# Performance work log

Measured on AMD Instinct MI355X. Metric: run time of the kernel, lower is better.

## Reference

```python
import jax, jax.numpy as jnp
import numpy as np

N = 2048; C_IN = 2; H = 32; EMB = 16; OUT = 1; HORIZON = 12
B = 32; T = 16

def setup_inputs() -> dict:
    key = jax.random.key(0)
    ks = jax.random.split(key, 10)
    s = 0.05
    return {
        "x":  jax.random.normal(ks[0], (B, T, N, C_IN), dtype=jnp.float32),
        "E1": jax.random.normal(ks[1], (N, EMB), dtype=jnp.float32) * 0.1,
        "E2": jax.random.normal(ks[2], (N, EMB), dtype=jnp.float32) * 0.1,
        "Wx": jax.random.normal(ks[3], (C_IN, 4 * H), dtype=jnp.float32) * s,
        "bx": jnp.zeros((4 * H,), dtype=jnp.float32),
        "Wh": jax.random.normal(ks[4], (H, 4 * H), dtype=jnp.float32) * s,
        "bh": jnp.zeros((4 * H,), dtype=jnp.float32),
        "Wp": jax.random.normal(ks[5], (H, OUT * HORIZON), dtype=jnp.float32) * s,
        "bp": jnp.zeros((OUT * HORIZON,), dtype=jnp.float32),
    }

def reference(x, E1, E2, Wx, bx, Wh, bh, Wp, bp):
    Bb, Tt, Nn, _ = x.shape
    # adaptive adjacency: softmax(relu(E1 @ E2^T)) over last dim  [N,N]
    A = jax.nn.softmax(jax.nn.relu(E1 @ E2.T), axis=-1)

    def step(carry, xt):
        h, c = carry  # [B,N,H]
        # fused graph-conv gates: (A @ xt) Wx + (A @ h) Wh + biases -> [B,N,4H]
        gates = (jnp.einsum('ij,bjc->bic', A, xt) @ Wx + bx
                 + jnp.einsum('ij,bjh->bih', A, h) @ Wh + bh)
        i, f, o, g = jnp.split(gates, 4, axis=-1)
        i = jax.nn.sigmoid(i); f = jax.nn.sigmoid(f); o = jax.nn.sigmoid(o)
        g = jnp.tanh(g)
        c_t = f * c + i * g
        h_t = o * jnp.tanh(c_t)
        return (h_t, c_t), None

    h0 = jnp.zeros((Bb, Nn, H), dtype=x.dtype)
    c0 = jnp.zeros((Bb, Nn, H), dtype=x.dtype)
    (h_last, _), _ = jax.lax.scan(step, (h0, c0), jnp.transpose(x, (1, 0, 2, 3)))
    out = h_last @ Wp + bp                      # [B,N,horizon*out]
    out = out.reshape(Bb, Nn, HORIZON, OUT)
    return jnp.transpose(out, (0, 2, 1, 3))     # [B,horizon,N,out]
```

## Files before the change

kernel.cpp:

```cpp
#include <hip/hip_runtime.h>
#include <hip/hip_bf16.h>
#include <cstddef>
#include <cstdint>

#define NN 2048
#define CIN 2
#define HH 32
#define EMB 16
#define HOR 12
#define BB 32
#define TT 16
#define GC 128
#define XCOLS 1024
#define HCOLS 1024

#define ATILE_STRIDE 65536
#define BTILE_STRIDE 32768
#define LOPLANE 2097152

typedef __attribute__((ext_vector_type(8))) _Float16 f16x8;
typedef __attribute__((ext_vector_type(16))) float f32x16;

__device__ __forceinline__ void load_lds16(const void* g, void* l) {
    __builtin_amdgcn_global_load_lds(
        (const __attribute__((address_space(1))) void*)g,
        (__attribute__((address_space(3))) void*)l, 16, 0, 0);
}

__global__ __launch_bounds__(256) void e2_transpose(const float* __restrict__ E2,
                                                    float* __restrict__ E2T) {
    const int idx = blockIdx.x * 256 + threadIdx.x;
    const int k = idx >> 11;
    const int j = idx & 2047;
    E2T[idx] = E2[j * EMB + k];
}

__global__ __launch_bounds__(256) void precompute(const float* __restrict__ E1,
                                                  const float* __restrict__ E2T,
                                                  const float* __restrict__ x,
                                                  const float* __restrict__ Wx,
                                                  const float* __restrict__ bx,
                                                  const float* __restrict__ Wh,
                                                  const float* __restrict__ bh,
                                                  _Float16* __restrict__ A2,
                                                  _Float16* __restrict__ B2x,
                                                  _Float16* __restrict__ W16,
                                                  float* __restrict__ Wxr,
                                                  float* __restrict__ bfold) {
    const int blk = blockIdx.x;
    const int tid = threadIdx.x;

    if (blk < 512) {
        const int i = blk * 4 + (tid >> 6);
        const int l = tid & 63;
        float e1[EMB];
#pragma unroll
        for (int k = 0; k < EMB; ++k) e1[k] = E1[i * EMB + k];

        float s[32];
#pragma unroll
        for (int c = 0; c < 32; ++c) s[c] = 0.f;
#pragma unroll
        for (int k = 0; k < EMB; ++k) {
            const float ek = e1[k];
            const float* p = E2T + k * 2048 + l;
#pragma unroll
            for (int c = 0; c < 32; ++c) s[c] = fmaf(ek, p[c * 64], s[c]);
        }
        float mx = 0.f;
#pragma unroll
        for (int c = 0; c < 32; ++c) { s[c] = fmaxf(s[c], 0.f); mx = fmaxf(mx, s[c]); }
#pragma unroll
        for (int off = 32; off > 0; off >>= 1) mx = fmaxf(mx, __shfl_xor(mx, off, 64));
        float sum = 0.f;
#pragma unroll
        for (int c = 0; c < 32; ++c) { s[c] = expf(s[c] - mx); sum += s[c]; }
#pragma unroll
        for (int off = 32; off > 0; off >>= 1) sum += __shfl_xor(sum, off, 64);
        const float inv = 1.0f / sum;
        const int chb = (l >> 3);
        const int e   = l & 7;
#pragma unroll
        for (int c = 0; c < 32; ++c)
            A2[((size_t)(c * 8 + chb) * 2048 + i) * 8 + e] = (_Float16)(s[c] * inv);
    } else if (blk < 512 + 1024) {
        const int idx = (blk - 512) * 256 + tid;
        const int col = idx & 1023;
        const int jc  = idx >> 10;
        const int bt  = col >> 1;
        const int c   = col & 1;
        const float* xp = x + ((size_t)bt * NN + jc * 8) * CIN + c;
        f16x8 vh, vl;
#pragma unroll
        for (int e = 0; e < 8; ++e) {
            const float v = xp[e * CIN];
            const _Float16 hi = (_Float16)v;
            vh[e] = hi;
            vl[e] = (_Float16)(v - (float)hi);
        }
        const size_t base = ((size_t)jc * 1024 + col) * 8;
        *(f16x8*)(B2x + base) = vh;
        *(f16x8*)(B2x + base + LOPLANE) = vl;
    } else {
#pragma unroll
        for (int r = 0; r < 32; ++r) {
            const int idx = r * 256 + tid;
            const int e  = idx & 7;
            const int ln = (idx >> 3) & 63;
            const int gq = (idx >> 9) & 3;
            const int kh = (idx >> 11) & 1;
            const int k  = kh * 16 + (ln >> 5) * 8 + e;
            const int ch = gq * 32 + (ln & 31);
            const float v = Wh[k * GC + (ch & 3) * HH + (ch >> 2)];
            const _Float16 hi = (_Float16)v;
            W16[idx] = hi;
            W16[8192 + idx] = (_Float16)(v - (float)hi);
        }
        {
            const int idx = tid;
            const int c = idx >> 7, rem = idx & 127;
            const int h = rem >> 2, g = rem & 3;
            Wxr[idx] = Wx[c * GC + g * HH + h];
        }
        if (tid < 128) {
            const int h = tid >> 2, g = tid & 3;
            bfold[tid] = bx[g * HH + h] + bh[g * HH + h];
        }
    }
}

template <int NPROD, int GATE>
__global__ __launch_bounds__(512, 2) void gemm_fused(const _Float16* __restrict__ A2,
                                                     const _Float16* __restrict__ B2,
                                                     float* __restrict__ Cout,
                                                     const float* __restrict__ AX,
                                                     const _Float16* __restrict__ W16,
                                                     const float* __restrict__ Wxr,
                                                     const float* __restrict__ bfold,
                                                     float* __restrict__ cst,
                                                     float* __restrict__ h32,
                                                     _Float16* __restrict__ hTout,
                                                     int t, int last) {
    constexpr int SUBS   = (NPROD == 1) ? 2 : 1;
    constexpr int NT     = 64 / SUBS;
    constexpr int SUBBUF = 4096 + NPROD * 8192;
    constexpr int BUF    = SUBS * SUBBUF;
    constexpr int NBUF   = (NPROD == 1) ? 4 : 6;
    constexpr int PCH    = 256 + NPROD * 512;
    constexpr int NG     = (SUBS * PCH) / 64;
    constexpr int GMAX   = 3;
    constexpr int STAGE_SZ = NBUF * BUF;
    constexpr int SMEMSZ = GATE ? (STAGE_SZ + 1024 + 512 + 2048) : STAGE_SZ;
    __shared__ __align__(16) char smem[SMEMSZ];

    const int tid  = threadIdx.x;
    const int w    = tid >> 6;
    const int lane = tid & 63;

    const int wg = blockIdx.x;
    const int x8 = wg & 7;
    const int s  = wg >> 3;
    const int mb = (x8 >> 1) * 8 + (s & 7);
    const int nb = (x8 & 1) * 4 + (s >> 3);
    const int m0 = mb * 64;
    const int n0 = nb * 128;

    float* wxr_s = nullptr; float* bfl_s = nullptr; float* axs = nullptr;
    if constexpr (GATE) {
        wxr_s = (float*)(smem + STAGE_SZ);
        bfl_s = (float*)(smem + STAGE_SZ + 1024);
        axs   = (float*)(smem + STAGE_SZ + 1536);
        const int b0c = nb * 4;
        if (tid < 64) *(float4*)&wxr_s[tid * 4] = *(const float4*)&Wxr[tid * 4];
        if (tid < 32) *(float4*)&bfl_s[tid * 4] = *(const float4*)&bfold[tid * 4];
        axs[tid] = AX[(size_t)(m0 + (tid & 63)) * XCOLS +
                      ((b0c + (tid >> 7)) * TT + t) * CIN + ((tid >> 6) & 1)];
    }

    const _Float16* gp[GMAX];
    int lbase[GMAX];
    int adv[GMAX];
    bool val[GMAX];
#pragma unroll
    for (int i = 0; i < GMAX; ++i) {
        const int g = w + 8 * i;
        val[i] = (g < NG);
        const int gg = val[i] ? g : 0;
        const int cid  = gg * 64 + lane;
        const int cid0 = gg * 64;
        const int su  = cid / PCH,  r  = cid  - su * PCH;
        const int su0 = cid0 / PCH, r0 = cid0 - su0 * PCH;
        if (r < 256) {
            gp[i]  = A2 + ((size_t)((su * 4 + (r >> 6)) * 2048) + m0 + (r & 63)) * 8;
            adv[i] = SUBS * ATILE_STRIDE;
        } else {
            const int r2 = r - 256;
            gp[i]  = B2 + (size_t)(r2 >> 9) * LOPLANE
                        + ((size_t)((su * 4 + ((r2 & 511) >> 7)) * 1024) + n0 + (r2 & 127)) * 8;
            adv[i] = SUBS * BTILE_STRIDE;
        }
        lbase[i] = su0 * SUBBUF + (r0 < 256 ? r0 * 16 : 4096 + (r0 - 256) * 16);
    }

    const int lrow = lane & 31, lg = lane >> 5;
    const int mi = w >> 2;
    const int gq = w & 3;
    const int wc = gq * 32;
    const int aoff0 = lg * 1024 + (mi * 32 + lrow) * 16;
    const int aoff1 = 2048 + lg * 1024 + (mi * 32 + lrow) * 16;
    const int boff0 = 4096 + lg * 2048 + (wc + lrow) * 16;
    const int boff1 = 4096 + 4096 + lg * 2048 + (wc + lrow) * 16;
    const int gqk = w & 3;
    const int kvk = w >> 2;
    const int subb  = kvk * SUBBUF;
    const int a00 = subb + lg * 1024 + lrow * 16;
    const int a01 = subb + 2048 + lg * 1024 + lrow * 16;
    const int a10 = a00 + 512;
    const int a11 = a01 + 512;
    const int bk0 = subb + 4096 + lg * 2048 + (gqk * 32 + lrow) * 16;
    const int bk1 = bk0 + 4096;

    f32x16 acc0 = (f32x16)(0.0f), acc1 = (f32x16)(0.0f);
    f32x16 acc2 = (f32x16)(0.0f), acc3 = (f32x16)(0.0f);

#define STAGE(BUFI) do {                                                       \
    char* lb = smem + (BUFI) * BUF;                                            \
    _Pragma("unroll")                                                          \
    for (int i = 0; i < GMAX; ++i) if (val[i]) {                               \
        load_lds16(gp[i], lb + lbase[i]);                                      \
        gp[i] += adv[i];                                                       \
    }                                                                          \
} while (0)

#define VMW(NHI, NLO) do {                                                     \
    if (w < 4) asm volatile("s_waitcnt vmcnt(" #NHI ")" ::: "memory");         \
    else       asm volatile("s_waitcnt vmcnt(" #NLO ")" ::: "memory");         \
} while (0)

#define BAR() do {                                                             \
    __builtin_amdgcn_s_barrier();                                              \
    asm volatile("" ::: "memory");                                             \
} while (0)

#define COMPUTE1(BUFI) do {                                                    \
    const char* st = smem + (BUFI) * BUF;                                      \
    f16x8 fa00 = *(const f16x8*)(st + a00);                                    \
    f16x8 fa01 = *(const f16x8*)(st + a01);                                    \
    f16x8 fa10 = *(const f16x8*)(st + a10);                                    \
    f16x8 fa11 = *(const f16x8*)(st + a11);                                    \
    f16x8 fb0  = *(const f16x8*)(st + bk0);                                    \
    f16x8 fb1  = *(const f16x8*)(st + bk1);                                    \
    acc0 = __builtin_amdgcn_mfma_f32_32x32x16_f16(fa00, fb0, acc0, 0, 0, 0);   \
    acc1 = __builtin_amdgcn_mfma_f32_32x32x16_f16(fa01, fb1, acc1, 0, 0, 0);   \
    acc2 = __builtin_amdgcn_mfma_f32_32x32x16_f16(fa10, fb0, acc2, 0, 0, 0);   \
    acc3 = __builtin_amdgcn_mfma_f32_32x32x16_f16(fa11, fb1, acc3, 0, 0, 0);   \
} while (0)

#define COMPUTE2(BUFI) do {                                                    \
    const char* st = smem + (BUFI) * BUF;                                      \
    f16x8 fa0 = *(const f16x8*)(st + aoff0);                                   \
    f16x8 fa1 = *(const f16x8*)(st + aoff1);                                   \
    f16x8 fb0 = *(const f16x8*)(st + boff0);                                   \
    f16x8 fb1 = *(const f16x8*)(st + boff1);                                   \
    acc0 = __builtin_amdgcn_mfma_f32_32x32x16_f16(fa0, fb0, acc0, 0, 0, 0);    \
    acc1 = __builtin_amdgcn_mfma_f32_32x32x16_f16(fa1, fb1, acc1, 0, 0, 0);    \
    f16x8 fc0 = *(const f16x8*)(st + boff0 + 8192);                            \
    f16x8 fc1 = *(const f16x8*)(st + boff1 + 8192);                            \
    acc0 = __builtin_amdgcn_mfma_f32_32x32x16_f16(fa0, fc0, acc0, 0, 0, 0);    \
    acc1 = __builtin_amdgcn_mfma_f32_32x32x16_f16(fa1, fc1, acc1, 0, 0, 0);    \
} while (0)

    if constexpr (NPROD == 1) {
        STAGE(0);
        STAGE(1);
#pragma unroll 1
        for (int it = 0; it < NT - 2; ++it) {
            STAGE((it + 2) & 3);
            asm volatile("s_waitcnt vmcnt(6)" ::: "memory");
            BAR();
            COMPUTE1(it & 3);
        }
        asm volatile("s_waitcnt vmcnt(3)" ::: "memory");
        BAR();
        COMPUTE1((NT - 2) & 3);
        asm volatile("s_waitcnt vmcnt(0)" ::: "memory");
        BAR();
        COMPUTE1((NT - 1) & 3);
    } else {
        STAGE(0);
        STAGE(1);
        STAGE(2);
        int bs = 3, bc = 0;
#pragma unroll 1
        for (int it = 0; it < NT - 3; ++it) {
            STAGE(bs);
            VMW(9, 6);
            BAR();
            COMPUTE2(bc);
            bs = (bs == 5) ? 0 : bs + 1;
            bc = (bc == 5) ? 0 : bc + 1;
        }
        VMW(6, 4);
        BAR();
        COMPUTE2(bc); bc = (bc == 5) ? 0 : bc + 1;
        VMW(3, 2);
        BAR();
        COMPUTE2(bc); bc = (bc == 5) ? 0 : bc + 1;
        asm volatile("s_waitcnt vmcnt(0)" ::: "memory");
        BAR();
        COMPUTE2(bc);
    }
#undef STAGE
#undef VMW
#undef BAR
#undef COMPUTE1
#undef COMPUTE2

    if constexpr (NPROD == 1) {
        f32x16 fin0, fin1;
#pragma unroll
        for (int r = 0; r < 16; ++r) { fin0[r] = acc0[r] + acc1[r]; fin1[r] = acc2[r] + acc3[r]; }
        {
            float* red = (float*)smem;
            if (kvk == 1) {
                float* rp0 = red + (gqk * 2 + 0) * 1024 + lane;
                float* rp1 = red + (gqk * 2 + 1) * 1024 + lane;
#pragma unroll
                for (int r = 0; r < 16; ++r) { rp0[r * 64] = fin0[r]; rp1[r * 64] = fin1[r]; }
            }
            __syncthreads();
            if (kvk == 0) {
                const float* rp0 = red + (gqk * 2 + 0) * 1024 + lane;
                const float* rp1 = red + (gqk * 2 + 1) * 1024 + lane;
#pragma unroll
                for (int r = 0; r < 16; ++r) { fin0[r] += rp0[r * 64]; fin1[r] += rp1[r * 64]; }
            }
            __syncthreads();
        }

        if constexpr (!GATE) {
            if (kvk == 0) {
                const int colg = n0 + gqk * 32 + lrow;
#pragma unroll
                for (int r = 0; r < 16; ++r) {
                    const int rp = (r & 3) + 8 * (r >> 2) + 4 * lg;
                    Cout[(size_t)(m0 + rp) * XCOLS + colg]      = fin0[r];
                    Cout[(size_t)(m0 + 32 + rp) * XCOLS + colg] = fin1[r];
                }
            }
        } else {
            f16x8 wbh0 = *(const f16x8*)(W16 + ((size_t)(0 * 4 + gq) * 64 + lane) * 8);
            f16x8 wbh1 = *(const f16x8*)(W16 + ((size_t)(1 * 4 + gq) * 64 + lane) * 8);
            f16x8 wbl0 = *(const f16x8*)(W16 + 8192 + ((size_t)(0 * 4 + gq) * 64 + lane) * 8);
            f16x8 wbl1 = *(const f16x8*)(W16 + 8192 + ((size_t)(1 * 4 + gq) * 64 + lane) * 8);

            _Float16* ahh = (_Float16*)smem;
            _Float16* ahl = (_Float16*)(smem + 17408);
            if (kvk == 0) {
                const int colw = gqk * 32 + lrow;
#pragma unroll
                for (int r = 0; r < 16; ++r) {
                    const int rp = (r & 3) + 8 * (r >> 2) + 4 * lg;
                    const float v0 = fin0[r];
                    const _Float16 h0 = (_Float16)v0;
                    ahh[rp * 136 + colw] = h0;
                    ahl[rp * 136 + colw] = (_Float16)(v0 - (float)h0);
                    const float v1 = fin1[r];
                    const _Float16 h1 = (_Float16)v1;
                    ahh[(32 + rp) * 136 + colw] = h1;
                    ahl[(32 + rp) * 136 + colw] = (_Float16)(v1 - (float)h1);
                }
            }
            __syncthreads();

            f32x16 g0 = (f32x16)(0.0f), g1 = (f32x16)(0.0f);
            f32x16 g2 = (f32x16)(0.0f), g3 = (f32x16)(0.0f);
#define GATEB(ACC, b) do {                                                         \
    const int arow = (mi * 32 + lrow) * 136 + (b) * 32 + lg * 8;                   \
    f16x8 fh0 = *(const f16x8*)(ahh + arow);                                       \
    f16x8 fl0 = *(const f16x8*)(ahl + arow);                                       \
    f16x8 fh1 = *(const f16x8*)(ahh + arow + 16);                                  \
    f16x8 fl1 = *(const f16x8*)(ahl + arow + 16);                                  \
    ACC = __builtin_amdgcn_mfma_f32_32x32x16_f16(fh0, wbh0, ACC, 0, 0, 0);         \
    ACC = __builtin_amdgcn_mfma_f32_32x32x16_f16(fh0, wbl0, ACC, 0, 0, 0);         \
    ACC = __builtin_amdgcn_mfma_f32_32x32x16_f16(fl0, wbh0, ACC, 0, 0, 0);         \
    ACC = __builtin_amdgcn_mfma_f32_32x32x16_f16(fh1, wbh1, ACC, 0, 0, 0);         \
    ACC = __builtin_amdgcn_mfma_f32_32x32x16_f16(fh1, wbl1, ACC, 0, 0, 0);         \
    ACC = __builtin_amdgcn_mfma_f32_32x32x16_f16(fl1, wbh1, ACC, 0, 0, 0);         \
} while (0)
            GATEB(g0, 0); GATEB(g1, 1); GATEB(g2, 2); GATEB(g3, 3);
#undef GATEB

            float* gl = (float*)(smem + 34816);
            const int nl2 = tid & 63;
            const int hb  = (tid >> 6) * 4;
            const int b0c = nb * 4;
            const int nd  = m0 + nl2;
            const size_t ntbase = ((size_t)((nd >> 5) * 4 + ((nd >> 3) & 3)) * 1024) * 8 + (nd & 7);

#define POINT(ACC, bi) do {                                                        \
    _Pragma("unroll")                                                              \
    for (int r = 0; r < 16; ++r) {                                                 \
        const int rp = (r & 3) + 8 * (r >> 2) + 4 * lg;                            \
        gl[(mi * 32 + rp) * 132 + gq * 32 + lrow] = ACC[r];                        \
    }                                                                              \
    __syncthreads();                                                               \
    {                                                                              \
        const float ax0 = axs[(bi) * 128 + nl2];                                   \
        const float ax1 = axs[(bi) * 128 + 64 + nl2];                              \
        const int bb = b0c + (bi);                                                 \
        const size_t off = (size_t)nd * HCOLS + bb * HH + hb;                      \
        const float4 co = *(const float4*)(cst + off);                             \
        const float cold[4] = {co.x, co.y, co.z, co.w};                            \
        float cn[4], hn[4];                                                        \
        _Pragma("unroll")                                                          \
        for (int p = 0; p < 4; ++p) {                                              \
            const int hh = hb + p;                                                 \
            const float4 gt = *(const float4*)(gl + nl2 * 132 + hh * 4);           \
            const float a0 = gt.x + bfl_s[hh*4+0] + ax0*wxr_s[hh*4+0] + ax1*wxr_s[128+hh*4+0]; \
            const float a1 = gt.y + bfl_s[hh*4+1] + ax0*wxr_s[hh*4+1] + ax1*wxr_s[128+hh*4+1]; \
            const float a2 = gt.z + bfl_s[hh*4+2] + ax0*wxr_s[hh*4+2] + ax1*wxr_s[128+hh*4+2]; \
            const float a3 = gt.w + bfl_s[hh*4+3] + ax0*wxr_s[hh*4+3] + ax1*wxr_s[128+hh*4+3]; \
            const float i_ = 1.0f / (1.0f + expf(-a0));                            \
            const float f_ = 1.0f / (1.0f + expf(-a1));                            \
            const float o_ = 1.0f / (1.0f + expf(-a2));                            \
            const float g_ = tanhf(a3);                                            \
            const float ct = f_ * cold[p] + i_ * g_;                               \
            cn[p] = ct;                                                            \
            hn[p] = o_ * tanhf(ct);                                                \
        }                                                                          \
        *(float4*)(cst + off) = make_float4(cn[0], cn[1], cn[2], cn[3]);           \
        if (last) *(float4*)(h32 + off) = make_float4(hn[0], hn[1], hn[2], hn[3]); \
        _Pragma("unroll")                                                          \
        for (int p = 0; p < 4; ++p)                                                \
            hTout[ntbase + (size_t)(bb * HH + hb + p) * 8] = (_Float16)hn[p];      \
    }                                                                              \
    __syncthreads();                                                               \
} while (0)
            POINT(g0, 0); POINT(g1, 1); POINT(g2, 2); POINT(g3, 3);
#undef POINT
        }
    } else {
        const int colg = n0 + wc + lrow;
#pragma unroll
        for (int r = 0; r < 16; ++r) {
            const int rp = (r & 3) + 8 * (r >> 2) + 4 * lg;
            Cout[(size_t)(m0 + mi * 32 + rp) * XCOLS + colg] = acc0[r] + acc1[r];
        }
    }
}

__global__ __launch_bounds__(256) void gate_update(const float* __restrict__ AX,
                                                   const float* __restrict__ Wxr,
                                                   const float* __restrict__ bfold,
                                                   float* __restrict__ c,
                                                   float* __restrict__ h32,
                                                   _Float16* __restrict__ hT) {
    const int n0 = blockIdx.x * 64;
    const int b0 = blockIdx.y * 4;
    const int tid = threadIdx.x;
    __shared__ float wxr[256];
    __shared__ float bfl[128];
    __shared__ float axs[2][64];

    if (tid < 64)  *(float4*)&wxr[tid * 4] = *(const float4*)&Wxr[tid * 4];
    if (tid < 32)  *(float4*)&bfl[tid * 4] = *(const float4*)&bfold[tid * 4];

    const int nl = tid & 63;
    const int hq = tid >> 6;

    const int nd = n0 + nl;
    const size_t ntbase = ((size_t)((nd >> 5) * 4 + ((nd >> 3) & 3)) * 1024) * 8 + (nd & 7);

#pragma unroll 1
    for (int bi = 0; bi < 4; ++bi) {
        const int b = b0 + bi;
        if (bi) __syncthreads();
        if (tid < 128) {
            const int which = tid >> 6, nls = tid & 63;
            axs[which][nls] = AX[(size_t)(n0 + nls) * XCOLS + (b * TT + 0) * CIN + which];
        }
        __syncthreads();

        const float ax0 = axs[0][nl], ax1 = axs[1][nl];
        float cn[8], hn[8];
#pragma unroll
        for (int u = 0; u < 8; ++u) {
            const int h = hq * 8 + u;
            float a0 = bfl[h * 4 + 0] + ax0 * wxr[h * 4 + 0] + ax1 * wxr[128 + h * 4 + 0];
            float a1 = bfl[h * 4 + 1] + ax0 * wxr[h * 4 + 1] + ax1 * wxr[128 + h * 4 + 1];
            float a2 = bfl[h * 4 + 2] + ax0 * wxr[h * 4 + 2] + ax1 * wxr[128 + h * 4 + 2];
            float a3 = bfl[h * 4 + 3] + ax0 * wxr[h * 4 + 3] + ax1 * wxr[128 + h * 4 + 3];
            const float i_ = 1.0f / (1.0f + expf(-a0));
            const float f_ = 1.0f / (1.0f + expf(-a1));
            const float o_ = 1.0f / (1.0f + expf(-a2));
            const float g_ = tanhf(a3);
            const float ct = i_ * g_;
            (void)f_;
            cn[u] = ct;
            hn[u] = o_ * tanhf(ct);
        }
        const size_t off = (size_t)nd * HCOLS + b * HH + hq * 8;
        *(float4*)(c + off)       = make_float4(cn[0], cn[1], cn[2], cn[3]);
        *(float4*)(c + off + 4)   = make_float4(cn[4], cn[5], cn[6], cn[7]);
        *(float4*)(h32 + off)     = make_float4(hn[0], hn[1], hn[2], hn[3]);
        *(float4*)(h32 + off + 4) = make_float4(hn[4], hn[5], hn[6], hn[7]);
#pragma unroll
        for (int u = 0; u < 8; ++u)
            hT[ntbase + (size_t)(b * HH + hq * 8 + u) * 8] = (_Float16)hn[u];
    }
}

__global__ __launch_bounds__(256) void head_kernel(const float* __restrict__ h,
                                                   const float* __restrict__ Wp,
                                                   const float* __restrict__ bp,
                                                   float* __restrict__ out) {
    const int idx = blockIdx.x * 256 + threadIdx.x;
    const int b = idx >> 11;
    const int n = idx & (NN - 1);
    float hv[HH];
    const float* hp = h + (size_t)n * HCOLS + b * HH;
#pragma unroll
    for (int k = 0; k < HH; ++k) hv[k] = hp[k];
#pragma unroll
    for (int th = 0; th < HOR; ++th) {
        float acc = bp[th];
#pragma unroll
        for (int k = 0; k < HH; ++k) acc += hv[k] * Wp[k * HOR + th];
        out[((size_t)b * HOR + th) * NN + n] = acc;
    }
}

extern "C" void kernel_launch(void* const* d_in, const int* in_sizes, int n_in,
                              void* d_out, int out_size, void* d_ws, size_t ws_size,
                              hipStream_t stream) {
    const float* x  = (const float*)d_in[0];
    const float* E1 = (const float*)d_in[1];
    const float* E2 = (const float*)d_in[2];
    const float* Wx = (const float*)d_in[3];
    const float* bx = (const float*)d_in[4];
    const float* Wh = (const float*)d_in[5];
    const float* bh = (const float*)d_in[6];
    const float* Wp = (const float*)d_in[7];
    const float* bp = (const float*)d_in[8];

    char* ws = (char*)d_ws;
    _Float16* A2  = (_Float16*)(ws);
    _Float16* B2x = (_Float16*)(ws + ( 8ull << 20));
    _Float16* hT0 = (_Float16*)(ws + (16ull << 20));
    _Float16* hT1 = (_Float16*)(ws + (20ull << 20));
    float* AX   = (float*)(ws + (24ull << 20));
    float* cst  = (float*)(ws + (32ull << 20));
    float* h32  = (float*)(ws + (40ull << 20));
    float* Wxr  = (float*)(ws + (48ull << 20) + 65536);
    float* bfold= (float*)(ws + (48ull << 20) + 131072);
    _Float16* W16 = (_Float16*)(ws + (48ull << 20) + 262144);
    float* E2T  = (float*)(ws + (48ull << 20) + 524288);
    _Float16* hTb[2] = {hT0, hT1};

    e2_transpose<<<128, 256, 0, stream>>>(E2, E2T);

    precompute<<<512 + 1024 + 1, 256, 0, stream>>>(E1, E2T, x, Wx, bx, Wh, bh,
                                                   A2, B2x, W16, Wxr, bfold);

    gemm_fused<2, 0><<<256, 512, 0, stream>>>(A2, B2x, AX, nullptr, nullptr, nullptr,
                                              nullptr, nullptr, nullptr, nullptr, 0, 0);

    gate_update<<<dim3(NN / 64, BB / 4), 256, 0, stream>>>(AX, Wxr, bfold,
                                                           cst, h32, hTb[0]);
    for (int t = 1; t < TT; ++t) {
        gemm_fused<1, 1><<<256, 512, 0, stream>>>(A2, hTb[(t + 1) & 1], nullptr, AX,
                                                  W16, Wxr, bfold, cst, h32,
                                                  hTb[t & 1], t, t == TT - 1 ? 1 : 0);
    }

    head_kernel<<<(BB * NN) / 256, 256, 0, stream>>>(h32, Wp, bp, (float*)d_out);
}
```

Baseline: 536.6 us.

## Replace per-timestep kernel launches with a persistent cooperative recurrent kernel

Splits the templated GEMM into a standalone input-projection kernel and a persistent cooperative kernel that loops over the 15 recurrent timesteps. Timesteps are separated by grid.sync instead of separate launches, and the Wh fragments and constant tables are loaded once. The aim is to remove launch gaps and repeated prologue work between steps. In exchange it adds grid-wide barrier cost, and launch bounds move to one block per CU, which relies on all 256 blocks being co-resident.

```diff
diff --git a/kernel.cpp b/kernel.cpp
--- a/kernel.cpp
+++ b/kernel.cpp
@@ -1,7 +1,10 @@
 #include <hip/hip_runtime.h>
 #include <hip/hip_bf16.h>
+#include <hip/hip_cooperative_groups.h>
 #include <cstddef>
 #include <cstdint>
+
+namespace cg = cooperative_groups;
 
 #define NN 2048
 #define CIN 2
@@ -129,29 +132,16 @@
     }
 }
 
-template <int NPROD, int GATE>
-__global__ __launch_bounds__(512, 2) void gemm_fused(const _Float16* __restrict__ A2,
-                                                     const _Float16* __restrict__ B2,
-                                                     float* __restrict__ Cout,
-                                                     const float* __restrict__ AX,
-                                                     const _Float16* __restrict__ W16,
-                                                     const float* __restrict__ Wxr,
-                                                     const float* __restrict__ bfold,
-                                                     float* __restrict__ cst,
-                                                     float* __restrict__ h32,
-                                                     _Float16* __restrict__ hTout,
-                                                     int t, int last) {
-    constexpr int SUBS   = (NPROD == 1) ? 2 : 1;
-    constexpr int NT     = 64 / SUBS;
-    constexpr int SUBBUF = 4096 + NPROD * 8192;
-    constexpr int BUF    = SUBS * SUBBUF;
-    constexpr int NBUF   = (NPROD == 1) ? 4 : 6;
-    constexpr int PCH    = 256 + NPROD * 512;
-    constexpr int NG     = (SUBS * PCH) / 64;
+__global__ __launch_bounds__(512, 2) void gemm_x(const _Float16* __restrict__ A2,
+                                                 const _Float16* __restrict__ B2,
+                                                 float* __restrict__ Cout) {
+    constexpr int NT     = 64;
+    constexpr int SUBBUF = 20480;
+    constexpr int BUF    = 20480;
+    constexpr int PCH    = 1280;
+    constexpr int NG     = 20;
     constexpr int GMAX   = 3;
-    constexpr int STAGE_SZ = NBUF * BUF;
-    constexpr int SMEMSZ = GATE ? (STAGE_SZ + 1024 + 512 + 2048) : STAGE_SZ;
-    __shared__ __align__(16) char smem[SMEMSZ];
+    __shared__ __align__(16) char smem[6 * BUF];
 
     const int tid  = threadIdx.x;
     const int w    = tid >> 6;
@@ -165,18 +155,6 @@
     const int m0 = mb * 64;
     const int n0 = nb * 128;
 
-    float* wxr_s = nullptr; float* bfl_s = nullptr; float* axs = nullptr;
-    if constexpr (GATE) {
-        wxr_s = (float*)(smem + STAGE_SZ);
-        bfl_s = (float*)(smem + STAGE_SZ + 1024);
-        axs   = (float*)(smem + STAGE_SZ + 1536);
-        const int b0c = nb * 4;
-        if (tid < 64) *(float4*)&wxr_s[tid * 4] = *(const float4*)&Wxr[tid * 4];
-        if (tid < 32) *(float4*)&bfl_s[tid * 4] = *(const float4*)&bfold[tid * 4];
-        axs[tid] = AX[(size_t)(m0 + (tid & 63)) * XCOLS +
-                      ((b0c + (tid >> 7)) * TT + t) * CIN + ((tid >> 6) & 1)];
-    }
-
     const _Float16* gp[GMAX];
     int lbase[GMAX];
     int adv[GMAX];
@@ -188,18 +166,16 @@
         const int gg = val[i] ? g : 0;
         const int cid  = gg * 64 + lane;
         const int cid0 = gg * 64;
-        const int su  = cid / PCH,  r  = cid  - su * PCH;
-        const int su0 = cid0 / PCH, r0 = cid0 - su0 * PCH;
-        if (r < 256) {
-            gp[i]  = A2 + ((size_t)((su * 4 + (r >> 6)) * 2048) + m0 + (r & 63)) * 8;
-            adv[i] = SUBS * ATILE_STRIDE;
+        if (cid < 256) {
+            gp[i]  = A2 + ((size_t)((cid >> 6) * 2048) + m0 + (cid & 63)) * 8;
+            adv[i] = ATILE_STRIDE;
         } else {
-            const int r2 = r - 256;
+            const int r2 = cid - 256;
             gp[i]  = B2 + (size_t)(r2 >> 9) * LOPLANE
-                        + ((size_t)((su * 4 + ((r2 & 511) >> 7)) * 1024) + n0 + (r2 & 127)) * 8;
-            adv[i] = SUBS * BTILE_STRIDE;
-        }
-        lbase[i] = su0 * SUBBUF + (r0 < 256 ? r0 * 16 : 4096 + (r0 - 256) * 16);
+                        + ((size_t)(((r2 & 511) >> 7) * 1024) + n0 + (r2 & 127)) * 8;
+            adv[i] = BTILE_STRIDE;
+        }
+        lbase[i] = (cid0 < 256) ? cid0 * 16 : 4096 + (cid0 - 256) * 16;
     }
 
     const int lrow = lane & 31, lg = lane >> 5;
@@ -210,18 +186,8 @@
     const int aoff1 = 2048 + lg * 1024 + (mi * 32 + lrow) * 16;
     const int boff0 = 4096 + lg * 2048 + (wc + lrow) * 16;
     const int boff1 = 4096 + 4096 + lg * 2048 + (wc + lrow) * 16;
-    const int gqk = w & 3;
-    const int kvk = w >> 2;
-    const int subb  = kvk * SUBBUF;
-    const int a00 = subb + lg * 1024 + lrow * 16;
-    const int a01 = subb + 2048 + lg * 1024 + lrow * 16;
-    const int a10 = a00 + 512;
-    const int a11 = a01 + 512;
-    const int bk0 = subb + 4096 + lg * 2048 + (gqk * 32 + lrow) * 16;
-    const int bk1 = bk0 + 4096;
 
     f32x16 acc0 = (f32x16)(0.0f), acc1 = (f32x16)(0.0f);
-    f32x16 acc2 = (f32x16)(0.0f), acc3 = (f32x16)(0.0f);
 
 #define STAGE(BUFI) do {                                                       \
     char* lb = smem + (BUFI) * BUF;                                            \
@@ -235,6 +201,178 @@
 #define VMW(NHI, NLO) do {                                                     \
     if (w < 4) asm volatile("s_waitcnt vmcnt(" #NHI ")" ::: "memory");         \
     else       asm volatile("s_waitcnt vmcnt(" #NLO ")" ::: "memory");         \
+} while (0)
+
+#define BAR() do {                                                             \
+    __builtin_amdgcn_s_barrier();                                              \
+    asm volatile("" ::: "memory");                                             \
+} while (0)
+
+#define COMPUTE(BUFI) do {                                                     \
+    const char* st = smem + (BUFI) * BUF;                                      \
+    f16x8 fa0 = *(const f16x8*)(st + aoff0);                                   \
+    f16x8 fa1 = *(const f16x8*)(st + aoff1);                                   \
+    f16x8 fb0 = *(const f16x8*)(st + boff0);                                   \
+    f16x8 fb1 = *(const f16x8*)(st + boff1);                                   \
+    acc0 = __builtin_amdgcn_mfma_f32_32x32x16_f16(fa0, fb0, acc0, 0, 0, 0);    \
+    acc1 = __builtin_amdgcn_mfma_f32_32x32x16_f16(fa1, fb1, acc1, 0, 0, 0);    \
+    f16x8 fc0 = *(const f16x8*)(st + boff0 + 8192);                            \
+    f16x8 fc1 = *(const f16x8*)(st + boff1 + 8192);                            \
+    acc0 = __builtin_amdgcn_mfma_f32_32x32x16_f16(fa0, fc0, acc0, 0, 0, 0);    \
+    acc1 = __builtin_amdgcn_mfma_f32_32x32x16_f16(fa1, fc1, acc1, 0, 0, 0);    \
+} while (0)
+
+    STAGE(0);
+    STAGE(1);
+    STAGE(2);
+    int bs = 3, bc = 0;
+#pragma unroll 1
+    for (int it = 0; it < NT - 3; ++it) {
+        STAGE(bs);
+        VMW(9, 6);
+        BAR();
+        COMPUTE(bc);
+        bs = (bs == 5) ? 0 : bs + 1;
+        bc = (bc == 5) ? 0 : bc + 1;
+    }
+    VMW(6, 4);
+    BAR();
+    COMPUTE(bc); bc = (bc == 5) ? 0 : bc + 1;
+    VMW(3, 2);
+    BAR();
+    COMPUTE(bc); bc = (bc == 5) ? 0 : bc + 1;
+    asm volatile("s_waitcnt vmcnt(0)" ::: "memory");
+    BAR();
+    COMPUTE(bc);
+#undef STAGE
+#undef VMW
+#undef BAR
+#undef COMPUTE
+
+    const int colg = n0 + wc + lrow;
+#pragma unroll
+    for (int r = 0; r < 16; ++r) {
+        const int rp = (r & 3) + 8 * (r >> 2) + 4 * lg;
+        Cout[(size_t)(m0 + mi * 32 + rp) * XCOLS + colg] = acc0[r] + acc1[r];
+    }
+}
+
+__global__ __launch_bounds__(512, 1) void recurrent_loop(
+        const _Float16* __restrict__ A2,
+        _Float16* __restrict__ hTA,
+        _Float16* __restrict__ hTB,
+        const float* __restrict__ AX,
+        const _Float16* __restrict__ W16,
+        const float* __restrict__ Wxr,
+        const float* __restrict__ bfold,
+        float* __restrict__ cst,
+        float* __restrict__ h32) {
+    constexpr int SUBS   = 2;
+    constexpr int NT     = 32;
+    constexpr int SUBBUF = 12288;
+    constexpr int BUF    = 24576;
+    constexpr int PCH    = 768;
+    constexpr int NG     = 24;
+    constexpr int GMAX   = 3;
+    constexpr int STAGE_SZ = 98304;
+    __shared__ __align__(16) char smem[STAGE_SZ + 1024 + 512 + 2048];
+
+    const int tid  = threadIdx.x;
+    const int w    = tid >> 6;
+    const int lane = tid & 63;
+
+    const int wg = blockIdx.x;
+    const int x8 = wg & 7;
+    const int s  = wg >> 3;
+    const int mb = (x8 >> 1) * 8 + (s & 7);
+    const int nb = (x8 & 1) * 4 + (s >> 3);
+    const int m0 = mb * 64;
+    const int n0 = nb * 128;
+
+    float* wxr_s = (float*)(smem + STAGE_SZ);
+    float* bfl_s = (float*)(smem + STAGE_SZ + 1024);
+    float* axs   = (float*)(smem + STAGE_SZ + 1536);
+    const int b0c = nb * 4;
+    if (tid < 64) *(float4*)&wxr_s[tid * 4] = *(const float4*)&Wxr[tid * 4];
+    if (tid < 32) *(float4*)&bfl_s[tid * 4] = *(const float4*)&bfold[tid * 4];
+
+    size_t gofs[GMAX];
+    int lbase[GMAX];
+    int adv[GMAX];
+    bool isAg[GMAX];
+#pragma unroll
+    for (int i = 0; i < GMAX; ++i) {
+        const int g = w + 8 * i;
+        const int cid  = g * 64 + lane;
+        const int cid0 = g * 64;
+        const int su  = cid / PCH,  r  = cid  - su * PCH;
+        const int su0 = cid0 / PCH, r0 = cid0 - su0 * PCH;
+        if (r < 256) {
+            isAg[i] = true;
+            gofs[i] = ((size_t)((su * 4 + (r >> 6)) * 2048) + m0 + (r & 63)) * 8;
+            adv[i]  = SUBS * ATILE_STRIDE;
+        } else {
+            const int r2 = r - 256;
+            isAg[i] = false;
+            gofs[i] = ((size_t)((su * 4 + ((r2 & 511) >> 7)) * 1024) + n0 + (r2 & 127)) * 8;
+            adv[i]  = SUBS * BTILE_STRIDE;
+        }
+        lbase[i] = su0 * SUBBUF + (r0 < 256 ? r0 * 16 : 4096 + (r0 - 256) * 16);
+    }
+
+    const int lrow = lane & 31, lg = lane >> 5;
+    const int mi = w >> 2;
+    const int gq = w & 3;
+    const int gqk = w & 3;
+    const int kvk = w >> 2;
+    const int subb = kvk * SUBBUF;
+    const int a00 = subb + lg * 1024 + lrow * 16;
+    const int a01 = subb + 2048 + lg * 1024 + lrow * 16;
+    const int a10 = a00 + 512;
+    const int a11 = a01 + 512;
+    const int bk0 = subb + 4096 + lg * 2048 + (gqk * 32 + lrow) * 16;
+    const int bk1 = bk0 + 4096;
+
+    f16x8 wbh0 = *(const f16x8*)(W16 + ((size_t)(0 * 4 + gq) * 64 + lane) * 8);
+    f16x8 wbh1 = *(const f16x8*)(W16 + ((size_t)(1 * 4 + gq) * 64 + lane) * 8);
+    f16x8 wbl0 = *(const f16x8*)(W16 + 8192 + ((size_t)(0 * 4 + gq) * 64 + lane) * 8);
+    f16x8 wbl1 = *(const f16x8*)(W16 + 8192 + ((size_t)(1 * 4 + gq) * 64 + lane) * 8);
+
+    const int nl2 = tid & 63;
+    const int hb  = (tid >> 6) * 4;
+    const int nd  = m0 + nl2;
+    const size_t ntbase = ((size_t)((nd >> 5) * 4 + ((nd >> 3) & 3)) * 1024) * 8 + (nd & 7);
+
+    cg::grid_group grid = cg::this_grid();
+
+#pragma unroll 1
+    for (int t = 1; t < TT; ++t) {
+        if (t > 1) {
+            __threadfence();
+            grid.sync();
+        }
+        const _Float16* B2 = (t & 1) ? hTA : hTB;
+        _Float16* hTout    = (t & 1) ? hTB : hTA;
+        const int last = (t == TT - 1) ? 1 : 0;
+
+        axs[tid] = AX[(size_t)(m0 + (tid & 63)) * XCOLS +
+                      ((b0c + (tid >> 7)) * TT + t) * CIN + ((tid >> 6) & 1)];
+        asm volatile("s_waitcnt vmcnt(0)" ::: "memory");
+
+        const _Float16* gp[GMAX];
+#pragma unroll
+        for (int i = 0; i < GMAX; ++i) gp[i] = (isAg[i] ? A2 : B2) + gofs[i];
+
+        f32x16 acc0 = (f32x16)(0.0f), acc1 = (f32x16)(0.0f);
+        f32x16 acc2 = (f32x16)(0.0f), acc3 = (f32x16)(0.0f);
+
+#define STAGE(BUFI) do {                                                       \
+    char* lb = smem + (BUFI) * BUF;                                            \
+    _Pragma("unroll")                                                          \
+    for (int i = 0; i < GMAX; ++i) {                                           \
+        load_lds16(gp[i], lb + lbase[i]);                                      \
+        gp[i] += adv[i];                                                       \
+    }                                                                          \
 } while (0)
 
 #define BAR() do {                                                             \
@@ -256,21 +394,6 @@
     acc3 = __builtin_amdgcn_mfma_f32_32x32x16_f16(fa11, fb1, acc3, 0, 0, 0);   \
 } while (0)
 
-#define COMPUTE2(BUFI) do {                                                    \
-    const char* st = smem + (BUFI) * BUF;                                      \
-    f16x8 fa0 = *(const f16x8*)(st + aoff0);                                   \
-    f16x8 fa1 = *(const f16x8*)(st + aoff1);                                   \
-    f16x8 fb0 = *(const f16x8*)(st + boff0);                                   \
-    f16x8 fb1 = *(const f16x8*)(st + boff1);                                   \
-    acc0 = __builtin_amdgcn_mfma_f32_32x32x16_f16(fa0, fb0, acc0, 0, 0, 0);    \
-    acc1 = __builtin_amdgcn_mfma_f32_32x32x16_f16(fa1, fb1, acc1, 0, 0, 0);    \
-    f16x8 fc0 = *(const f16x8*)(st + boff0 + 8192);                            \
-    f16x8 fc1 = *(const f16x8*)(st + boff1 + 8192);                            \
-    acc0 = __builtin_amdgcn_mfma_f32_32x32x16_f16(fa0, fc0, acc0, 0, 0, 0);    \
-    acc1 = __builtin_amdgcn_mfma_f32_32x32x16_f16(fa1, fc1, acc1, 0, 0, 0);    \
-} while (0)
-
-    if constexpr (NPROD == 1) {
         STAGE(0);
         STAGE(1);
 #pragma unroll 1
@@ -286,37 +409,10 @@
         asm volatile("s_waitcnt vmcnt(0)" ::: "memory");
         BAR();
         COMPUTE1((NT - 1) & 3);
-    } else {
-        STAGE(0);
-        STAGE(1);
-        STAGE(2);
-        int bs = 3, bc = 0;
-#pragma unroll 1
-        for (int it = 0; it < NT - 3; ++it) {
-            STAGE(bs);
-            VMW(9, 6);
-            BAR();
-            COMPUTE2(bc);
-            bs = (bs == 5) ? 0 : bs + 1;
-            bc = (bc == 5) ? 0 : bc + 1;
-        }
-        VMW(6, 4);
-        BAR();
-        COMPUTE2(bc); bc = (bc == 5) ? 0 : bc + 1;
-        VMW(3, 2);
-        BAR();
-        COMPUTE2(bc); bc = (bc == 5) ? 0 : bc + 1;
-        asm volatile("s_waitcnt vmcnt(0)" ::: "memory");
-        BAR();
-        COMPUTE2(bc);
-    }
 #undef STAGE
-#undef VMW
 #undef BAR
 #undef COMPUTE1
-#undef COMPUTE2
-
-    if constexpr (NPROD == 1) {
+
         f32x16 fin0, fin1;
 #pragma unroll
         for (int r = 0; r < 16; ++r) { fin0[r] = acc0[r] + acc1[r]; fin1[r] = acc2[r] + acc3[r]; }
@@ -338,43 +434,27 @@
             __syncthreads();
         }
 
-        if constexpr (!GATE) {
-            if (kvk == 0) {
-                const int colg = n0 + gqk * 32 + lrow;
-#pragma unroll
-                for (int r = 0; r < 16; ++r) {
-                    const int rp = (r & 3) + 8 * (r >> 2) + 4 * lg;
-                    Cout[(size_t)(m0 + rp) * XCOLS + colg]      = fin0[r];
-                    Cout[(size_t)(m0 + 32 + rp) * XCOLS + colg] = fin1[r];
-                }
+        _Float16* ahh = (_Float16*)smem;
+        _Float16* ahl = (_Float16*)(smem + 17408);
+        if (kvk == 0) {
+            const int colw = gqk * 32 + lrow;
+#pragma unroll
+            for (int r = 0; r < 16; ++r) {
+                const int rp = (r & 3) + 8 * (r >> 2) + 4 * lg;
+                const float v0 = fin0[r];
+                const _Float16 h0 = (_Float16)v0;
+                ahh[rp * 136 + colw] = h0;
+                ahl[rp * 136 + colw] = (_Float16)(v0 - (float)h0);
+                const float v1 = fin1[r];
+                const _Float16 h1 = (_Float16)v1;
+                ahh[(32 + rp) * 136 + colw] = h1;
+                ahl[(32 + rp) * 136 + colw] = (_Float16)(v1 - (float)h1);
             }
-        } else {
-            f16x8 wbh0 = *(const f16x8*)(W16 + ((size_t)(0 * 4 + gq) * 64 + lane) * 8);
-            f16x8 wbh1 = *(const f16x8*)(W16 + ((size_t)(1 * 4 + gq) * 64 + lane) * 8);
-            f16x8 wbl0 = *(const f16x8*)(W16 + 8192 + ((size_t)(0 * 4 + gq) * 64 + lane) * 8);
-            f16x8 wbl1 = *(const f16x8*)(W16 + 8192 + ((size_t)(1 * 4 + gq) * 64 + lane) * 8);
-
-            _Float16* ahh = (_Float16*)smem;
-            _Float16* ahl = (_Float16*)(smem + 17408);
-            if (kvk == 0) {
-                const int colw = gqk * 32 + lrow;
-#pragma unroll
-                for (int r = 0; r < 16; ++r) {
-                    const int rp = (r & 3) + 8 * (r >> 2) + 4 * lg;
-                    const float v0 = fin0[r];
-                    const _Float16 h0 = (_Float16)v0;
-                    ahh[rp * 136 + colw] = h0;
-                    ahl[rp * 136 + colw] = (_Float16)(v0 - (float)h0);
-                    const float v1 = fin1[r];
-                    const _Float16 h1 = (_Float16)v1;
-                    ahh[(32 + rp) * 136 + colw] = h1;
-                    ahl[(32 + rp) * 136 + colw] = (_Float16)(v1 - (float)h1);
-                }
-            }
-            __syncthreads();
-
-            f32x16 g0 = (f32x16)(0.0f), g1 = (f32x16)(0.0f);
-            f32x16 g2 = (f32x16)(0.0f), g3 = (f32x16)(0.0f);
+        }
+        __syncthreads();
+
+        f32x16 g0 = (f32x16)(0.0f), g1 = (f32x16)(0.0f);
+        f32x16 g2 = (f32x16)(0.0f), g3 = (f32x16)(0.0f);
 #define GATEB(ACC, b) do {                                                         \
     const int arow = (mi * 32 + lrow) * 136 + (b) * 32 + lg * 8;                   \
     f16x8 fh0 = *(const f16x8*)(ahh + arow);                                       \
@@ -388,16 +468,10 @@
     ACC = __builtin_amdgcn_mfma_f32_32x32x16_f16(fh1, wbl1, ACC, 0, 0, 0);         \
     ACC = __builtin_amdgcn_mfma_f32_32x32x16_f16(fl1, wbh1, ACC, 0, 0, 0);         \
 } while (0)
-            GATEB(g0, 0); GATEB(g1, 1); GATEB(g2, 2); GATEB(g3, 3);
+        GATEB(g0, 0); GATEB(g1, 1); GATEB(g2, 2); GATEB(g3, 3);
 #undef GATEB
 
-            float* gl = (float*)(smem + 34816);
-            const int nl2 = tid & 63;
-            const int hb  = (tid >> 6) * 4;
-            const int b0c = nb * 4;
-            const int nd  = m0 + nl2;
-            const size_t ntbase = ((size_t)((nd >> 5) * 4 + ((nd >> 3) & 3)) * 1024) * 8 + (nd & 7);
-
+        float* gl = (float*)(smem + 34816);
 #define POINT(ACC, bi) do {                                                        \
     _Pragma("unroll")                                                              \
     for (int r = 0; r < 16; ++r) {                                                 \
@@ -437,16 +511,8 @@
     }                                                                              \
     __syncthreads();                                                               \
 } while (0)
-            POINT(g0, 0); POINT(g1, 1); POINT(g2, 2); POINT(g3, 3);
+        POINT(g0, 0); POINT(g1, 1); POINT(g2, 2); POINT(g3, 3);
 #undef POINT
-        }
-    } else {
-        const int colg = n0 + wc + lrow;
-#pragma unroll
-        for (int r = 0; r < 16; ++r) {
-            const int rp = (r & 3) + 8 * (r >> 2) + 4 * lg;
-            Cout[(size_t)(m0 + mi * 32 + rp) * XCOLS + colg] = acc0[r] + acc1[r];
-        }
     }
 }
 
@@ -556,22 +622,28 @@
     float* bfold= (float*)(ws + (48ull << 20) + 131072);
     _Float16* W16 = (_Float16*)(ws + (48ull << 20) + 262144);
     float* E2T  = (float*)(ws + (48ull << 20) + 524288);
-    _Float16* hTb[2] = {hT0, hT1};
 
     e2_transpose<<<128, 256, 0, stream>>>(E2, E2T);
 
     precompute<<<512 + 1024 + 1, 256, 0, stream>>>(E1, E2T, x, Wx, bx, Wh, bh,
                                                    A2, B2x, W16, Wxr, bfold);
 
-    gemm_fused<2, 0><<<256, 512, 0, stream>>>(A2, B2x, AX, nullptr, nullptr, nullptr,
-                                              nullptr, nullptr, nullptr, nullptr, 0, 0);
+    gemm_x<<<256, 512, 0, stream>>>(A2, B2x, AX);
 
     gate_update<<<dim3(NN / 64, BB / 4), 256, 0, stream>>>(AX, Wxr, bfold,
-                                                           cst, h32, hTb[0]);
-    for (int t = 1; t < TT; ++t) {
-        gemm_fused<1, 1><<<256, 512, 0, stream>>>(A2, hTb[(t + 1) & 1], nullptr, AX,
-                                                  W16, Wxr, bfold, cst, h32,
-                                                  hTb[t & 1], t, t == TT - 1 ? 1 : 0);
+                                                           cst, h32, hT0);
+
+    {
+        const _Float16* A2c = A2;
+        const float* AXc = AX;
+        const _Float16* W16c = W16;
+        const float* Wxrc = Wxr;
+        const float* bfoldc = bfold;
+        void* cargs[] = {(void*)&A2c, (void*)&hT0, (void*)&hT1, (void*)&AXc,
+                         (void*)&W16c, (void*)&Wxrc, (void*)&bfoldc,
+                         (void*)&cst, (void*)&h32};
+        hipLaunchCooperativeKernel(recurrent_loop, dim3(256), dim3(512),
+                                   cargs, 0, stream);
     }
 
     head_kernel<<<(BB * NN) / 256, 256, 0, stream>>>(h32, Wp, bp, (float*)d_out);
```

Measured after the change: 1.554 ms. 2.9x slower.
